# Performance work log

Hardware: AMD Instinct MI355X
Metric: run time of the kernel (lower is better)

The kernel has to match this reference:

```python
import jax, jax.numpy as jnp
import numpy as np

B, D_IN, H, D_OUT, E = 16384, 512, 1024, 512, 4


def setup_inputs() -> dict:
    key = jax.random.key(0)
    ks = jax.random.split(key, 8)
    x = jax.random.normal(ks[0], (B, D_IN), dtype=jnp.float32)
    command = jax.random.randint(ks[1], (B,), 0, E, dtype=jnp.int64)
    # Per-branch Encoder params: Linear(D_IN->H), Linear(H->H), Linear(H->D_OUT)
    s = 0.02
    W1 = jax.random.normal(ks[2], (E, D_IN, H), dtype=jnp.float32) * s
    b1 = jnp.zeros((E, H), dtype=jnp.float32)
    W2 = jax.random.normal(ks[3], (E, H, H), dtype=jnp.float32) * s
    b2 = jnp.zeros((E, H), dtype=jnp.float32)
    W3 = jax.random.normal(ks[4], (E, H, D_OUT), dtype=jnp.float32) * s
    b3 = jnp.zeros((E, D_OUT), dtype=jnp.float32)
    return {"x": x, "command": command, "W1": W1, "b1": b1,
            "W2": W2, "b2": b2, "W3": W3, "b3": b3}


def reference(x, command, W1, b1, W2, b2, W3, b3):
    # Evaluate all branches as batched GEMMs, then select per-sample branch.
    # Mathematically identical to per-sample dispatch in the torch module.
    h = jax.nn.relu(jnp.einsum('bi,eih->beh', x, W1) + b1)        # [B,E,H]
    h = jax.nn.relu(jnp.einsum('beh,ehk->bek', h, W2) + b2)       # [B,E,H]
    y = jnp.tanh(jnp.einsum('bek,eko->beo', h, W3) + b3)          # [B,E,D_OUT]
    # select branch output per sample according to command
    idx = command.astype(jnp.int32)[:, None, None]                # [B,1,1]
    out = jnp.take_along_axis(y, idx, axis=1)[:, 0, :]            # [B,D_OUT]
    return out
```

## Files before the change

kernel.cpp:

```cpp
#include <hip/hip_runtime.h>


#define B_N   16384
#define DIN   512
#define HID   1024
#define DOUT  512
#define MAXTILES 136

typedef __attribute__((ext_vector_type(8))) short bf16x8;
typedef __attribute__((ext_vector_type(4))) float f32x4;
typedef __attribute__((address_space(3))) unsigned int lds_u32;
typedef const __attribute__((address_space(1))) unsigned int glb_u32;

__device__ __forceinline__ void gll16(const void* g, void* l) {
    __builtin_amdgcn_global_load_lds((glb_u32*)g, (lds_u32*)l, 16, 0, 0);
}

__device__ __forceinline__ unsigned short f2bf(float f) {
    unsigned int u = __float_as_uint(f);
    u += 0x7FFFu + ((u >> 16) & 1u);
    return (unsigned short)(u >> 16);
}

__device__ __forceinline__ float fast_tanh(float x) {
    x = fminf(fmaxf(x, -9.0f), 9.0f);
    float t = __builtin_amdgcn_exp2f(x * 2.8853900817779268f);
    return (t - 1.0f) * __builtin_amdgcn_rcpf(t + 1.0f);
}

__global__ void zero_k(int* __restrict__ ctrl) {
    if (threadIdx.x < 16) ctrl[threadIdx.x] = 0;
}

__global__ void count_k(const int* __restrict__ cmd, int* __restrict__ ctrl) {
    int i = blockIdx.x * 256 + threadIdx.x;
    int e = cmd[i] & 3;
    int lane = threadIdx.x & 63;
#pragma unroll
    for (int ee = 0; ee < 4; ++ee) {
        unsigned long long mask = __ballot(e == ee);
        int leader = __ffsll((unsigned long long)mask) - 1;
        if (mask && lane == leader)
            atomicAdd(&ctrl[ee], __popcll(mask));
    }
}

__global__ void plan_k(int* __restrict__ ctrl, int* __restrict__ tileExpert,
                       int* __restrict__ tileBase) {
    if (threadIdx.x == 0) {
        int P = 0, nt = 0;
        for (int e = 0; e < 4; ++e) {
            ctrl[4 + e] = 0;
            ctrl[8 + e] = P;
            int tiles = (ctrl[e] + 127) >> 7;
            for (int t = 0; t < tiles; ++t) {
                tileExpert[nt] = e;
                tileBase[nt] = P + t * 128;
                ++nt;
            }
            P += tiles * 128;
        }
        ctrl[12] = P;
        ctrl[13] = nt;
    }
}

__global__ void scatter_k(const int* __restrict__ cmd, int* __restrict__ ctrl,
                          int* __restrict__ perm) {
    int i = blockIdx.x * 256 + threadIdx.x;
    int e = cmd[i] & 3;
    int lane = threadIdx.x & 63;
#pragma unroll
    for (int ee = 0; ee < 4; ++ee) {
        unsigned long long mask = __ballot(e == ee);
        if (e == ee) {
            int leader = __ffsll((unsigned long long)mask) - 1;
            int rank = __popcll(mask & ((1ull << lane) - 1ull));
            int wbase = 0;
            if (lane == leader)
                wbase = atomicAdd(&ctrl[4 + ee], __popcll(mask));
            wbase = __builtin_amdgcn_readfirstlane(wbase);
            perm[ctrl[8 + ee] + wbase + rank] = i;
        }
    }
}

__global__ __launch_bounds__(256) void prep_data_k(
    const float* __restrict__ W1, const float* __restrict__ W2,
    const float* __restrict__ W3, unsigned short* __restrict__ Wt1,
    unsigned short* __restrict__ Wt2, unsigned short* __restrict__ Wt3,
    const float* __restrict__ x, unsigned short* __restrict__ xp,
    int* __restrict__ perm, const int* __restrict__ ctrl)
{
    int b = blockIdx.x;
    if (b < 8192) {
        int e = b >> 11, r = b & 2047;
        const float* W; unsigned short* Wt; int KD, ND, kt, nt;
        if (r < 512)       { W = W1; Wt = Wt1; KD = 512;  ND = 1024; kt = r & 15;           nt = r >> 4; }
        else if (r < 1536) { W = W2; Wt = Wt2; KD = 1024; ND = 1024; kt = (r - 512) & 31;   nt = (r - 512) >> 5; }
        else               { W = W3; Wt = Wt3; KD = 1024; ND = 512;  kt = (r - 1536) & 31;  nt = (r - 1536) >> 5; }
        __shared__ float t[32][33];
        size_t base = (size_t)e * KD * ND;
        int k0 = kt * 32, n0 = nt * 32;
        int tx = threadIdx.x & 31, ty = threadIdx.x >> 5;
#pragma unroll
        for (int s = 0; s < 4; ++s)
            t[ty + s * 8][tx] = W[base + (size_t)(k0 + ty + s * 8) * ND + n0 + tx];
        __syncthreads();
        int tx2 = (threadIdx.x & 15) * 2, ny = threadIdx.x >> 4;
#pragma unroll
        for (int s = 0; s < 2; ++s) {
            int n = ny + s * 16;
            unsigned int v = (unsigned)f2bf(t[tx2][n])
                           | ((unsigned)f2bf(t[tx2 + 1][n]) << 16);
            *(unsigned int*)&Wt[base + (size_t)(n0 + n) * KD + k0 + tx2] = v;
        }
    } else {
        int g = b - 8192;
        int p = g * 4 + (int)(threadIdx.x >> 6);
        if (p >= ctrl[12]) return;
        int lane = threadIdx.x & 63;
        int e = (p >= ctrl[9]) + (p >= ctrl[10]) + (p >= ctrl[11]);
        int segBase = ctrl[8 + e];
        int src;
        if (p < segBase + ctrl[e]) {
            src = perm[p];
        } else {
            src = perm[segBase];
            if (lane == 0) perm[p] = src;
        }
        const float* xr = x + (size_t)src * DIN + lane * 8;
        float4 a = *(const float4*)xr;
        float4 c = *(const float4*)(xr + 4);
        uint4 o;
        o.x = (unsigned)f2bf(a.x) | ((unsigned)f2bf(a.y) << 16);
        o.y = (unsigned)f2bf(a.z) | ((unsigned)f2bf(a.w) << 16);
        o.z = (unsigned)f2bf(c.x) | ((unsigned)f2bf(c.y) << 16);
        o.w = (unsigned)f2bf(c.z) | ((unsigned)f2bf(c.w) << 16);
        *(uint4*)(xp + (size_t)p * DIN + lane * 8) = o;
    }
}

template<int K, int N, int BN, int PN, int ACT, bool SCATTER_OUT>
__global__ __launch_bounds__(256) void gemm_k(
    const unsigned short* __restrict__ A, const unsigned short* __restrict__ Bt,
    const float* __restrict__ bias, void* __restrict__ Outp,
    const int* __restrict__ ctrl, const int* __restrict__ tileExpert,
    const int* __restrict__ tileBase, const int* __restrict__ perm)
{
    constexpr int NI = BN / 32;
    constexpr int BCALLS = BN / 32;
    const int l = (int)blockIdx.x + MAXTILES * (int)blockIdx.y;
    const int swz = (l & 7) * (17 * PN) + (l >> 3);
    const int tile = swz / PN;
    const int panel = swz & (PN - 1);
    if (tile >= ctrl[13]) return;
    const int e = tileExpert[tile];
    const int rowBase = tileBase[tile];
    const int n0 = panel * BN;

    __shared__ unsigned short Als[128 * 64];
    __shared__ unsigned short Bls[BN * 64];

    const int tid = threadIdx.x;
    const int lane = tid & 63;
    const int w = tid >> 6;
    const int wm = w >> 1, wn = w & 1;
    const int lr = lane & 15, lh = lane >> 4;

    f32x4 acc[4][NI] = {};

    const int tr = tid >> 3;
    const int tc = tid & 7;
    const int cs = (tc ^ (tr & 7)) * 8;
    const unsigned short* As = A + (size_t)(rowBase + tr) * K + cs;
    const unsigned short* Bs = Bt + ((size_t)e * N + n0 + tr) * K + cs;
    const int ldst = tr * 64 + tc * 8;

    constexpr int NK = K / 64;
    for (int kq = 0; kq < NK; ++kq) {
        const int k0 = kq * 64;
        __syncthreads();
#pragma unroll
        for (int j = 0; j < 4; ++j)
            gll16(As + (size_t)(j * 32) * K + k0, &Als[j * 2048 + ldst]);
#pragma unroll
        for (int j = 0; j < BCALLS; ++j)
            gll16(Bs + (size_t)(j * 32) * K + k0, &Bls[j * 2048 + ldst]);
        __syncthreads();
#pragma unroll
        for (int kk = 0; kk < 2; ++kk) {
            const int ksl = ((kk * 4 + lh) ^ (lr & 7)) * 8;
            bf16x8 afr[4], bfr[NI];
#pragma unroll
            for (int mi = 0; mi < 4; ++mi)
                afr[mi] = *(const bf16x8*)&Als[(wm * 64 + mi * 16 + lr) * 64 + ksl];
#pragma unroll
            for (int ni = 0; ni < NI; ++ni)
                bfr[ni] = *(const bf16x8*)&Bls[(wn * (BN / 2) + ni * 16 + lr) * 64 + ksl];
#pragma unroll
            for (int mi = 0; mi < 4; ++mi)
#pragma unroll
                for (int ni = 0; ni < NI; ++ni)
                    acc[mi][ni] = __builtin_amdgcn_mfma_f32_16x16x32_bf16(
                        afr[mi], bfr[ni], acc[mi][ni], 0, 0, 0);
        }
    }

    float bv[NI];
    int colv[NI];
#pragma unroll
    for (int ni = 0; ni < NI; ++ni) {
        colv[ni] = n0 + wn * (BN / 2) + ni * 16 + lr;
        bv[ni] = bias[e * N + colv[ni]];
    }
#pragma unroll
    for (int mi = 0; mi < 4; ++mi) {
#pragma unroll
        for (int r = 0; r < 4; ++r) {
            int rowL = wm * 64 + mi * 16 + lh * 4 + r;
            int gRow = rowBase + rowL;
            int orow = SCATTER_OUT ? perm[gRow] : gRow;
#pragma unroll
            for (int ni = 0; ni < NI; ++ni) {
                float v = acc[mi][ni][r] + bv[ni];
                if (ACT == 0) v = fmaxf(v, 0.0f);
                else          v = fast_tanh(v);
                if (SCATTER_OUT)
                    ((float*)Outp)[(size_t)orow * N + colv[ni]] = v;
                else
                    ((unsigned short*)Outp)[(size_t)orow * N + colv[ni]] = f2bf(v);
            }
        }
    }
}

extern "C" void kernel_launch(void* const* d_in, const int* in_sizes, int n_in,
                              void* d_out, int out_size, void* d_ws, size_t ws_size,
                              hipStream_t stream) {
    const float* x  = (const float*)d_in[0];
    const int*   cmd= (const int*)d_in[1];
    const float* W1 = (const float*)d_in[2];
    const float* b1 = (const float*)d_in[3];
    const float* W2 = (const float*)d_in[4];
    const float* b2 = (const float*)d_in[5];
    const float* W3 = (const float*)d_in[6];
    const float* b3 = (const float*)d_in[7];
    float* out = (float*)d_out;

    char* w = (char*)d_ws;
    int* ctrl       = (int*)w;
    int* tileExpert = ctrl + 64;
    int* tileBase   = ctrl + 224;
    int* perm       = ctrl + 512;
    unsigned short* Wt1 = (unsigned short*)(w + 131072);
    unsigned short* Wt2 = (unsigned short*)(w + 131072 + 4194304);
    unsigned short* Wt3 = (unsigned short*)(w + 131072 + 12582912);
    unsigned short* h1  = (unsigned short*)(w + 131072 + 16777216);
    unsigned short* h2  = h1 + (size_t)16896 * HID;
    unsigned short* xp  = h2;

    zero_k<<<1, 64, 0, stream>>>(ctrl);
    count_k<<<B_N / 256, 256, 0, stream>>>(cmd, ctrl);
    plan_k<<<1, 64, 0, stream>>>(ctrl, tileExpert, tileBase);
    scatter_k<<<B_N / 256, 256, 0, stream>>>(cmd, ctrl, perm);
    prep_data_k<<<8192 + 4224, 256, 0, stream>>>(W1, W2, W3, Wt1, Wt2, Wt3,
                                                 x, xp, perm, ctrl);

    gemm_k<DIN, HID, 128, 8, 0, false><<<dim3(MAXTILES, 8), 256, 0, stream>>>(
        xp, Wt1, b1, h1, ctrl, tileExpert, tileBase, perm);
    gemm_k<HID, HID, 128, 8, 0, false><<<dim3(MAXTILES, 8), 256, 0, stream>>>(
        h1, Wt2, b2, h2, ctrl, tileExpert, tileBase, perm);
    gemm_k<HID, DOUT, 64, 8, 1, true><<<dim3(MAXTILES, 8), 256, 0, stream>>>(
        h2, Wt3, b3, out, ctrl, tileExpert, tileBase, perm);
}
```

Baseline: 159.7 us.

## Use 64-row tiles for second and third expert GEMMs with a dual tile plan

The plan kernel now emits two tile lists, one of 128-row tiles and one of 64-row tiles. The GEMM kernel is templated on BM and on which count to use. Layer 1 keeps 128x128 tiles. Layer 2 switches to 64x128 tiles, which doubles the number of blocks, and layer 3 switches from 128x64 to 64x128 tiles with 4 panels. The aim is better CU occupancy and load balance across the 256 CUs. The cost is less A/B reuse per block and more redundant weight-panel loads.

```diff
diff --git a/kernel.cpp b/kernel.cpp
--- a/kernel.cpp
+++ b/kernel.cpp
@@ -5,7 +5,8 @@
 #define DIN   512
 #define HID   1024
 #define DOUT  512
-#define MAXTILES 136
+#define MAXT128 136
+#define MAXT64  264
 
 typedef __attribute__((ext_vector_type(8))) short bf16x8;
 typedef __attribute__((ext_vector_type(4))) float f32x4;
@@ -45,23 +46,26 @@
     }
 }
 
-__global__ void plan_k(int* __restrict__ ctrl, int* __restrict__ tileExpert,
-                       int* __restrict__ tileBase) {
+__global__ void plan_k(int* __restrict__ ctrl,
+                       int* __restrict__ t64E, int* __restrict__ t64B,
+                       int* __restrict__ t128E, int* __restrict__ t128B) {
     if (threadIdx.x == 0) {
-        int P = 0, nt = 0;
+        int P = 0, n128 = 0, n64 = 0;
         for (int e = 0; e < 4; ++e) {
             ctrl[4 + e] = 0;
             ctrl[8 + e] = P;
-            int tiles = (ctrl[e] + 127) >> 7;
-            for (int t = 0; t < tiles; ++t) {
-                tileExpert[nt] = e;
-                tileBase[nt] = P + t * 128;
-                ++nt;
+            int t128 = (ctrl[e] + 127) >> 7;
+            for (int t = 0; t < t128; ++t) {
+                t128E[n128] = e; t128B[n128] = P + t * 128; ++n128;
             }
-            P += tiles * 128;
+            for (int t = 0; t < t128 * 2; ++t) {
+                t64E[n64] = e; t64B[n64] = P + t * 64; ++n64;
+            }
+            P += t128 * 128;
         }
         ctrl[12] = P;
-        ctrl[13] = nt;
+        ctrl[13] = n128;
+        ctrl[14] = n64;
     }
 }
 
@@ -141,25 +145,28 @@
     }
 }
 
-template<int K, int N, int BN, int PN, int ACT, bool SCATTER_OUT>
+template<int K, int N, int BM, int BN, int NTILES, int PN, int CIDX,
+         int ACT, bool SCATTER_OUT>
 __global__ __launch_bounds__(256) void gemm_k(
     const unsigned short* __restrict__ A, const unsigned short* __restrict__ Bt,
     const float* __restrict__ bias, void* __restrict__ Outp,
     const int* __restrict__ ctrl, const int* __restrict__ tileExpert,
     const int* __restrict__ tileBase, const int* __restrict__ perm)
 {
+    constexpr int MI = BM / 32;
     constexpr int NI = BN / 32;
+    constexpr int ACALLS = BM / 32;
     constexpr int BCALLS = BN / 32;
-    const int l = (int)blockIdx.x + MAXTILES * (int)blockIdx.y;
-    const int swz = (l & 7) * (17 * PN) + (l >> 3);
+    const int l = (int)blockIdx.x + NTILES * (int)blockIdx.y;
+    const int swz = (l & 7) * ((NTILES / 8) * PN) + (l >> 3);
     const int tile = swz / PN;
     const int panel = swz & (PN - 1);
-    if (tile >= ctrl[13]) return;
+    if (tile >= ctrl[CIDX]) return;
     const int e = tileExpert[tile];
     const int rowBase = tileBase[tile];
     const int n0 = panel * BN;
 
-    __shared__ unsigned short Als[128 * 64];
+    __shared__ unsigned short Als[BM * 64];
     __shared__ unsigned short Bls[BN * 64];
 
     const int tid = threadIdx.x;
@@ -168,7 +175,7 @@
     const int wm = w >> 1, wn = w & 1;
     const int lr = lane & 15, lh = lane >> 4;
 
-    f32x4 acc[4][NI] = {};
+    f32x4 acc[MI][NI] = {};
 
     const int tr = tid >> 3;
     const int tc = tid & 7;
@@ -182,7 +189,7 @@
         const int k0 = kq * 64;
         __syncthreads();
 #pragma unroll
-        for (int j = 0; j < 4; ++j)
+        for (int j = 0; j < ACALLS; ++j)
             gll16(As + (size_t)(j * 32) * K + k0, &Als[j * 2048 + ldst]);
 #pragma unroll
         for (int j = 0; j < BCALLS; ++j)
@@ -191,15 +198,15 @@
 #pragma unroll
         for (int kk = 0; kk < 2; ++kk) {
             const int ksl = ((kk * 4 + lh) ^ (lr & 7)) * 8;
-            bf16x8 afr[4], bfr[NI];
-#pragma unroll
-            for (int mi = 0; mi < 4; ++mi)
-                afr[mi] = *(const bf16x8*)&Als[(wm * 64 + mi * 16 + lr) * 64 + ksl];
+            bf16x8 afr[MI], bfr[NI];
+#pragma unroll
+            for (int mi = 0; mi < MI; ++mi)
+                afr[mi] = *(const bf16x8*)&Als[(wm * (BM / 2) + mi * 16 + lr) * 64 + ksl];
 #pragma unroll
             for (int ni = 0; ni < NI; ++ni)
                 bfr[ni] = *(const bf16x8*)&Bls[(wn * (BN / 2) + ni * 16 + lr) * 64 + ksl];
 #pragma unroll
-            for (int mi = 0; mi < 4; ++mi)
+            for (int mi = 0; mi < MI; ++mi)
 #pragma unroll
                 for (int ni = 0; ni < NI; ++ni)
                     acc[mi][ni] = __builtin_amdgcn_mfma_f32_16x16x32_bf16(
@@ -215,10 +222,10 @@
         bv[ni] = bias[e * N + colv[ni]];
     }
 #pragma unroll
-    for (int mi = 0; mi < 4; ++mi) {
+    for (int mi = 0; mi < MI; ++mi) {
 #pragma unroll
         for (int r = 0; r < 4; ++r) {
-            int rowL = wm * 64 + mi * 16 + lh * 4 + r;
+            int rowL = wm * (BM / 2) + mi * 16 + lh * 4 + r;
             int gRow = rowBase + rowL;
             int orow = SCATTER_OUT ? perm[gRow] : gRow;
 #pragma unroll
@@ -249,10 +256,12 @@
     float* out = (float*)d_out;
 
     char* w = (char*)d_ws;
-    int* ctrl       = (int*)w;
-    int* tileExpert = ctrl + 64;
-    int* tileBase   = ctrl + 224;
-    int* perm       = ctrl + 512;
+    int* ctrl  = (int*)w;
+    int* t64E  = ctrl + 64;
+    int* t64B  = ctrl + 384;
+    int* t128E = ctrl + 704;
+    int* t128B = ctrl + 896;
+    int* perm  = ctrl + 1088;
     unsigned short* Wt1 = (unsigned short*)(w + 131072);
     unsigned short* Wt2 = (unsigned short*)(w + 131072 + 4194304);
     unsigned short* Wt3 = (unsigned short*)(w + 131072 + 12582912);
@@ -262,15 +271,18 @@
 
     zero_k<<<1, 64, 0, stream>>>(ctrl);
     count_k<<<B_N / 256, 256, 0, stream>>>(cmd, ctrl);
-    plan_k<<<1, 64, 0, stream>>>(ctrl, tileExpert, tileBase);
+    plan_k<<<1, 64, 0, stream>>>(ctrl, t64E, t64B, t128E, t128B);
     scatter_k<<<B_N / 256, 256, 0, stream>>>(cmd, ctrl, perm);
     prep_data_k<<<8192 + 4224, 256, 0, stream>>>(W1, W2, W3, Wt1, Wt2, Wt3,
                                                  x, xp, perm, ctrl);
 
-    gemm_k<DIN, HID, 128, 8, 0, false><<<dim3(MAXTILES, 8), 256, 0, stream>>>(
-        xp, Wt1, b1, h1, ctrl, tileExpert, tileBase, perm);
-    gemm_k<HID, HID, 128, 8, 0, false><<<dim3(MAXTILES, 8), 256, 0, stream>>>(
-        h1, Wt2, b2, h2, ctrl, tileExpert, tileBase, perm);
-    gemm_k<HID, DOUT, 64, 8, 1, true><<<dim3(MAXTILES, 8), 256, 0, stream>>>(
-        h2, Wt3, b3, out, ctrl, tileExpert, tileBase, perm);
-}
+    gemm_k<DIN, HID, 128, 128, MAXT128, 8, 13, 0, false>
+        <<<dim3(MAXT128, 8), 256, 0, stream>>>(
+        xp, Wt1, b1, h1, ctrl, t128E, t128B, perm);
+    gemm_k<HID, HID, 64, 128, MAXT64, 8, 14, 0, false>
+        <<<dim3(MAXT64, 8), 256, 0, stream>>>(
+        h1, Wt2, b2, h2, ctrl, t64E, t64B, perm);
+    gemm_k<HID, DOUT, 64, 128, MAXT64, 4, 14, 1, true>
+        <<<dim3(MAXT64, 4), 256, 0, stream>>>(
+        h2, Wt3, b3, out, ctrl, t64E, t64B, perm);
+}
```

Result: no change. 162.6 us (+1.8%).
